# Optimization experiments

Measured on AMD Instinct MI355X. Metric: run time of the kernel, lower is better.

## Reference

```python
import jax, jax.numpy as jnp
import numpy as np

IMG_SIZE = 256
NUM_ANGLES = 180
NUM_DETECTORS = 363  # ceil(sqrt(2)*256)


def setup_inputs() -> dict:
    key = jax.random.key(0)
    x = jax.random.normal(key, (4, 1, IMG_SIZE, IMG_SIZE), dtype=jnp.float32)
    return {"x": x}


def _radon(x):
    # x: (B,1,H,W) -> sinogram (B,1,A,D). Faithful to RadonTransform.forward
    # (grid_sample rotate, sum rows, bilinear resize detector axis, align_corners=True).
    B, C, H, W = x.shape
    A, D = NUM_ANGLES, NUM_DETECTORS
    angles = jnp.linspace(0.0, np.pi * (1.0 - 1.0 / A), A, dtype=x.dtype)
    yc = jnp.linspace(-1.0, 1.0, H, dtype=x.dtype)
    xc = jnp.linspace(-1.0, 1.0, W, dtype=x.dtype)
    yy, xx = jnp.meshgrid(yc, xc, indexing='ij')          # (H,W)
    cos_t = jnp.cos(-angles)[:, None, None]               # (A,1,1)
    sin_t = jnp.sin(-angles)[:, None, None]
    gx = xx[None] * cos_t - yy[None] * sin_t              # (A,H,W) normalized x coord
    gy = xx[None] * sin_t + yy[None] * cos_t              # (A,H,W) normalized y coord
    # grid_sample bilinear, padding_mode='zeros', align_corners=True
    fx = (gx + 1.0) * 0.5 * (W - 1)
    fy = (gy + 1.0) * 0.5 * (H - 1)
    x0 = jnp.floor(fx).astype(jnp.int32); x1 = x0 + 1
    y0 = jnp.floor(fy).astype(jnp.int32); y1 = y0 + 1
    wx = fx - x0.astype(x.dtype)
    wy = fy - y0.astype(x.dtype)
    img = x[:, 0]                                         # (B,H,W)

    def tap(yi, xi):
        valid = (yi >= 0) & (yi < H) & (xi >= 0) & (xi < W)
        ycl = jnp.clip(yi, 0, H - 1)
        xcl = jnp.clip(xi, 0, W - 1)
        v = img[:, ycl, xcl]                              # (B,A,H,W)
        return jnp.where(valid[None], v, jnp.zeros((), x.dtype))

    sampled = (tap(y0, x0) * ((1 - wy) * (1 - wx))[None]
               + tap(y0, x1) * ((1 - wy) * wx)[None]
               + tap(y1, x0) * (wy * (1 - wx))[None]
               + tap(y1, x1) * (wy * wx)[None])           # (B,A,H,W)
    proj = sampled.sum(axis=2)                            # (B,A,W) sum along rows (dim=2)
    # F.interpolate to (A, D), bilinear, align_corners=True; angle axis is identity.
    pos = jnp.arange(D, dtype=x.dtype) * (W - 1) / (D - 1)
    p0 = jnp.floor(pos).astype(jnp.int32)
    p1 = jnp.minimum(p0 + 1, W - 1)
    w = pos - p0.astype(x.dtype)
    sino = proj[:, :, p0] * (1.0 - w) + proj[:, :, p1] * w  # (B,A,D)
    return sino[:, None]                                   # (B,1,A,D)


def reference(x):
    # CTForwardModel.forward(x, add_noise=False): noiseless sinogram = Radon(x)
    return _radon(x)
```

## Files before the change

### kernel.cpp

```cpp
#include <hip/hip_runtime.h>
#include <hip/hip_fp16.h>
#include <math.h>

#define IMG   256
#define NANG  180
#define NDET  363
#define PAD   3
#define PS    264
#define PSZ   (PS * PS)
#define TEX_BYTES ((size_t)2 * PSZ * 8)
#define PP_BYTES  ((size_t)NANG * 2 * IMG * 16)
#define WS_NEED   (TEX_BYTES + PP_BYTES)

__device__ __forceinline__ __half2 u2h2(unsigned u) {
    return *reinterpret_cast<__half2*>(&u);
}
__device__ __forceinline__ unsigned h22u(__half2 h) {
    return *reinterpret_cast<unsigned*>(&h);
}

__global__ __launch_bounds__(1024) void prep_kernel(const float* __restrict__ x,
                                                    uint2* __restrict__ ws) {
    __shared__ uint2 tile[32][33];
    const int tx = threadIdx.x, ty = threadIdx.y;
    const int px = blockIdx.x * 32 + tx;
    const int py = blockIdx.y * 32 + ty;
    const int ix = px - PAD, iy = py - PAD;

    uint2 t = make_uint2(0u, 0u);
    if ((unsigned)ix < IMG && (unsigned)iy < IMG) {
        const size_t o = (size_t)iy * IMG + ix;
        const __half2 lo = __floats2half2_rn(x[o],                 x[o + IMG * IMG]);
        const __half2 hi = __floats2half2_rn(x[o + 2 * IMG * IMG], x[o + 3 * IMG * IMG]);
        t.x = h22u(lo);
        t.y = h22u(hi);
    }
    if (px < PS && py < PS) ws[(size_t)py * PS + px] = t;
    tile[ty][tx] = t;
    __syncthreads();
    const int opx = blockIdx.y * 32 + tx;
    const int opy = blockIdx.x * 32 + ty;
    if (opx < PS && opy < PS)
        ws[(size_t)PSZ + (size_t)opy * PS + opx] = tile[tx][ty];
}

__global__ __launch_bounds__(512) void radon_main(const uint2* __restrict__ ws,
                                                  float4* __restrict__ proj_part) {
    const int a    = blockIdx.x;
    const int ih   = blockIdx.y >> 1;
    const int jh   = blockIdx.y & 1;
    const int lane = threadIdx.x & 63;
    const int wv   = threadIdx.x >> 6;
    const int jj   = lane & 15;
    const int ii4  = lane >> 4;
    const int j    = jh * 128 + wv * 16 + jj;

    const float ang = (float)a * 0.017453292519943295f;
    const float cs = cosf(ang);
    const float sn = -sinf(ang);

    const float xcj = -1.0f + (2.0f / 255.0f) * (float)j;
    const float fx0 = 127.5f * (xcj * cs + sn + 1.0f);
    const float dfx = -sn;
    const float fy0 = 127.5f * (xcj * sn - cs + 1.0f);
    const float dfy = cs;

    const bool swp = fabsf(sn) > fabsf(cs);
    const float rc0 = swp ? fx0 : fy0;  const float drow = swp ? dfx : dfy;
    const float cc0 = swp ? fy0 : fx0;  const float dcol = swp ? dfy : dfx;
    const uint2* __restrict__ base = ws + (swp ? PSZ : 0);

    float lo = 0.0f, hi = 255.0f;
    if (fabsf(drow) > 1e-5f) {
        const float t1 = (-1.5f - rc0) / drow, t2 = (256.5f - rc0) / drow;
        lo = fmaxf(lo, fminf(t1, t2));
        hi = fminf(hi, fmaxf(t1, t2));
    } else if (rc0 < -1.5f || rc0 > 256.5f) { lo = 1.0f; hi = 0.0f; }
    if (fabsf(dcol) > 1e-5f) {
        const float t1 = (-1.5f - cc0) / dcol, t2 = (256.5f - cc0) / dcol;
        lo = fmaxf(lo, fminf(t1, t2));
        hi = fminf(hi, fmaxf(t1, t2));
    } else if (cc0 < -1.5f || cc0 > 256.5f) { lo = 1.0f; hi = 0.0f; }

    const int ibase = ih * 128;
    int ilo_t = max((int)floorf(lo), ibase);
    int ihi_t = min((int)ceilf(hi), ibase + 127);
    ihi_t = min(ihi_t, 255);
    const int d0 = ilo_t - ibase - ii4;
    const int d1 = ihi_t - ibase - ii4;
    const int klo = max(0, (d0 + 3) >> 2);
    const int khi = min(31, d1 >> 2);

    float4 sum = make_float4(0.f, 0.f, 0.f, 0.f);
    #pragma unroll 4
    for (int k = klo; k <= khi; ++k) {
        const int i = ibase + ii4 + (k << 2);
        const float rc = fmaf((float)i, drow, rc0);
        const float cc = fmaf((float)i, dcol, cc0);
        const float rf = floorf(rc);
        const float cf = floorf(cc);
        const float wr = rc - rf;
        const float wc = cc - cf;
        const int idx = (int)fmaf(rf, (float)PS, cf) + (PAD * PS + PAD);

        const uint4 tr = *reinterpret_cast<const uint4*>(base + idx);
        const uint4 br = *reinterpret_cast<const uint4*>(base + idx + PS);

        const __half2 wc2 = __float2half2_rn(wc);
        const __half2 wr2 = __float2half2_rn(wr);

        const __half2 v00a = u2h2(tr.x), v00b = u2h2(tr.y);
        const __half2 v01a = u2h2(tr.z), v01b = u2h2(tr.w);
        const __half2 v10a = u2h2(br.x), v10b = u2h2(br.y);
        const __half2 v11a = u2h2(br.z), v11b = u2h2(br.w);

        const __half2 topa = __hfma2(wc2, __hsub2(v01a, v00a), v00a);
        const __half2 topb = __hfma2(wc2, __hsub2(v01b, v00b), v00b);
        const __half2 bota = __hfma2(wc2, __hsub2(v11a, v10a), v10a);
        const __half2 botb = __hfma2(wc2, __hsub2(v11b, v10b), v10b);
        const __half2 ra = __hfma2(wr2, __hsub2(bota, topa), topa);
        const __half2 rb = __hfma2(wr2, __hsub2(botb, topb), topb);

        sum.x += __low2float(ra);
        sum.y += __high2float(ra);
        sum.z += __low2float(rb);
        sum.w += __high2float(rb);
    }

    sum.x += __shfl_xor(sum.x, 16, 64);
    sum.y += __shfl_xor(sum.y, 16, 64);
    sum.z += __shfl_xor(sum.z, 16, 64);
    sum.w += __shfl_xor(sum.w, 16, 64);
    sum.x += __shfl_xor(sum.x, 32, 64);
    sum.y += __shfl_xor(sum.y, 32, 64);
    sum.z += __shfl_xor(sum.z, 32, 64);
    sum.w += __shfl_xor(sum.w, 32, 64);

    if (ii4 == 0) {
        proj_part[(size_t)(a * 2 + ih) * IMG + j] = sum;
    }
}

__global__ __launch_bounds__(384) void detect_kernel(const float4* __restrict__ proj_part,
                                                     float* __restrict__ out) {
    const int a = blockIdx.x;
    const int t = threadIdx.x;
    __shared__ float4 proj[IMG];
    if (t < IMG) {
        const float4 p0 = proj_part[(size_t)(a * 2 + 0) * IMG + t];
        const float4 p1 = proj_part[(size_t)(a * 2 + 1) * IMG + t];
        proj[t] = make_float4(p0.x + p1.x, p0.y + p1.y, p0.z + p1.z, p0.w + p1.w);
    }
    __syncthreads();
    if (t < NDET) {
        const float pos = (float)t * (255.0f / 362.0f);
        const float fp = floorf(pos);
        const int p0 = (int)fp;
        const int p1 = min(p0 + 1, IMG - 1);
        const float w = pos - fp;
        const float4 lo = proj[p0], hi = proj[p1];
        const size_t o = (size_t)a * NDET + t;
        out[o]                   = fmaf(w, hi.x - lo.x, lo.x);
        out[o + 1 * NANG * NDET] = fmaf(w, hi.y - lo.y, lo.y);
        out[o + 2 * NANG * NDET] = fmaf(w, hi.z - lo.z, lo.z);
        out[o + 3 * NANG * NDET] = fmaf(w, hi.w - lo.w, lo.w);
    }
}

__global__ __launch_bounds__(256) void radon_fallback(const float* __restrict__ x,
                                                      float* __restrict__ out) {
    const int blk = blockIdx.x;
    const int a = blk >> 2;
    const int b = blk & 3;
    const int j = threadIdx.x;
    const float* __restrict__ img = x + (size_t)b * (IMG * IMG);
    const float ang = (float)a * 0.017453292519943295f;
    const float cs = cosf(ang);
    const float sn = -sinf(ang);
    const float xcj = -1.0f + (2.0f / 255.0f) * (float)j;
    const float gx0 = xcj * cs;
    const float gy0 = xcj * sn;
    float sum = 0.0f;
    for (int i = 0; i < IMG; ++i) {
        const float yci = -1.0f + (2.0f / 255.0f) * (float)i;
        const float fx = (gx0 - yci * sn + 1.0f) * 127.5f;
        const float fy = (gy0 + yci * cs + 1.0f) * 127.5f;
        const float flx = floorf(fx), fly = floorf(fy);
        const int x0 = (int)flx, y0 = (int)fly;
        const float wx = fx - flx, wy = fy - fly;
        const bool vx0 = ((unsigned)x0 < IMG), vx1 = ((unsigned)(x0 + 1) < IMG);
        const bool vy0 = ((unsigned)y0 < IMG), vy1 = ((unsigned)(y0 + 1) < IMG);
        if (!((vx0 | vx1) & (vy0 | vy1))) continue;
        const int xc0 = min(max(x0, 0), IMG - 1), xc1 = min(max(x0 + 1, 0), IMG - 1);
        const int yc0 = min(max(y0, 0), IMG - 1), yc1 = min(max(y0 + 1, 0), IMG - 1);
        const float* r0 = img + yc0 * IMG;
        const float* r1 = img + yc1 * IMG;
        const float v00 = (vy0 && vx0) ? r0[xc0] : 0.0f;
        const float v01 = (vy0 && vx1) ? r0[xc1] : 0.0f;
        const float v10 = (vy1 && vx0) ? r1[xc0] : 0.0f;
        const float v11 = (vy1 && vx1) ? r1[xc1] : 0.0f;
        sum += (1.0f - wy) * ((1.0f - wx) * v00 + wx * v01)
             +         wy  * ((1.0f - wx) * v10 + wx * v11);
    }
    __shared__ float proj[IMG];
    proj[j] = sum;
    __syncthreads();
    for (int d = j; d < NDET; d += 256) {
        const float pos = (float)d * (255.0f / 362.0f);
        const float fp = floorf(pos);
        const int p0 = (int)fp;
        const int p1 = min(p0 + 1, IMG - 1);
        const float w = pos - fp;
        out[(size_t)b * (NANG * NDET) + a * NDET + d] = proj[p0] * (1.0f - w) + proj[p1] * w;
    }
}

extern "C" void kernel_launch(void* const* d_in, const int* in_sizes, int n_in,
                              void* d_out, int out_size, void* d_ws, size_t ws_size,
                              hipStream_t stream) {
    const float* x = (const float*)d_in[0];
    float* out = (float*)d_out;
    (void)in_sizes; (void)n_in; (void)out_size;

    if (ws_size >= WS_NEED) {
        uint2* tex = (uint2*)d_ws;
        float4* proj_part = (float4*)((char*)d_ws + TEX_BYTES);
        prep_kernel<<<dim3(9, 9), dim3(32, 32), 0, stream>>>(x, tex);
        radon_main<<<dim3(NANG, 4), dim3(512), 0, stream>>>(tex, proj_part);
        detect_kernel<<<dim3(NANG), dim3(384), 0, stream>>>(proj_part, out);
    } else {
        radon_fallback<<<dim3(NANG * 4), dim3(256), 0, stream>>>(x, out);
    }
}
```

Measured before the change: 31.42 us.

## Fuse prep, projection and detector stages into one cooperative kernel with grid syncs

Replaces the three-kernel sequence with a single cooperative kernel that runs texture preparation, the per-angle line integrals, and detector interpolation, separated by grid-wide syncs. The aim is to remove two kernel launch gaps and their inter-kernel drain/fill overhead. It adds a host occupancy query on every call and grid.sync costs, and falls back to the old three launches if cooperative launch is not possible.

```diff
diff --git a/kernel.cpp b/kernel.cpp
--- a/kernel.cpp
+++ b/kernel.cpp
@@ -1,6 +1,9 @@
 #include <hip/hip_runtime.h>
+#include <hip/hip_cooperative_groups.h>
 #include <hip/hip_fp16.h>
 #include <math.h>
+
+namespace cg = cooperative_groups;
 
 #define IMG   256
 #define NANG  180
@@ -19,38 +22,12 @@
     return *reinterpret_cast<unsigned*>(&h);
 }
 
-__global__ __launch_bounds__(1024) void prep_kernel(const float* __restrict__ x,
-                                                    uint2* __restrict__ ws) {
-    __shared__ uint2 tile[32][33];
-    const int tx = threadIdx.x, ty = threadIdx.y;
-    const int px = blockIdx.x * 32 + tx;
-    const int py = blockIdx.y * 32 + ty;
-    const int ix = px - PAD, iy = py - PAD;
-
-    uint2 t = make_uint2(0u, 0u);
-    if ((unsigned)ix < IMG && (unsigned)iy < IMG) {
-        const size_t o = (size_t)iy * IMG + ix;
-        const __half2 lo = __floats2half2_rn(x[o],                 x[o + IMG * IMG]);
-        const __half2 hi = __floats2half2_rn(x[o + 2 * IMG * IMG], x[o + 3 * IMG * IMG]);
-        t.x = h22u(lo);
-        t.y = h22u(hi);
-    }
-    if (px < PS && py < PS) ws[(size_t)py * PS + px] = t;
-    tile[ty][tx] = t;
-    __syncthreads();
-    const int opx = blockIdx.y * 32 + tx;
-    const int opy = blockIdx.x * 32 + ty;
-    if (opx < PS && opy < PS)
-        ws[(size_t)PSZ + (size_t)opy * PS + opx] = tile[tx][ty];
-}
-
-__global__ __launch_bounds__(512) void radon_main(const uint2* __restrict__ ws,
-                                                  float4* __restrict__ proj_part) {
-    const int a    = blockIdx.x;
-    const int ih   = blockIdx.y >> 1;
-    const int jh   = blockIdx.y & 1;
-    const int lane = threadIdx.x & 63;
-    const int wv   = threadIdx.x >> 6;
+
+__device__ __forceinline__ void main_phase(const uint2* __restrict__ ws,
+                                           float4* __restrict__ proj_part,
+                                           int a, int ih, int jh, int tid) {
+    const int lane = tid & 63;
+    const int wv   = tid >> 6;
     const int jj   = lane & 15;
     const int ii4  = lane >> 4;
     const int j    = jh * 128 + wv * 16 + jj;
@@ -83,7 +60,7 @@
     } else if (cc0 < -1.5f || cc0 > 256.5f) { lo = 1.0f; hi = 0.0f; }
 
     const int ibase = ih * 128;
-    int ilo_t = max((int)floorf(lo), ibase);
+    const int ilo_t = max((int)floorf(lo), ibase);
     int ihi_t = min((int)ceilf(hi), ibase + 127);
     ihi_t = min(ihi_t, 255);
     const int d0 = ilo_t - ibase - ii4;
@@ -139,6 +116,108 @@
     if (ii4 == 0) {
         proj_part[(size_t)(a * 2 + ih) * IMG + j] = sum;
     }
+}
+
+__global__ __launch_bounds__(512, 6) void radon_fused(const float* __restrict__ x,
+                                                      uint2* __restrict__ tex,
+                                                      float4* __restrict__ proj_part,
+                                                      float* __restrict__ out) {
+    cg::grid_group grid = cg::this_grid();
+    const int bid = blockIdx.x;
+    const int tid = threadIdx.x;
+
+    __shared__ uint2 s_tile[16][33];
+    __shared__ float4 s_proj[IMG];
+
+    if (bid < 9 * 17) {
+        const int bx = bid % 9, by = bid / 9;
+        const int tx = tid & 31, ty = tid >> 5;
+        const int px = bx * 32 + tx;
+        const int py = by * 16 + ty;
+        const int ix = px - PAD, iy = py - PAD;
+
+        uint2 t = make_uint2(0u, 0u);
+        if ((unsigned)ix < IMG && (unsigned)iy < IMG) {
+            const size_t o = (size_t)iy * IMG + ix;
+            const __half2 lo = __floats2half2_rn(x[o],                 x[o + IMG * IMG]);
+            const __half2 hi = __floats2half2_rn(x[o + 2 * IMG * IMG], x[o + 3 * IMG * IMG]);
+            t.x = h22u(lo);
+            t.y = h22u(hi);
+        }
+        if (px < PS && py < PS) tex[(size_t)py * PS + px] = t;
+        s_tile[ty][tx] = t;
+        __syncthreads();
+        const int u_local = tid >> 4;
+        const int v_local = tid & 15;
+        const int u = bx * 32 + u_local;
+        const int v = by * 16 + v_local;
+        if (u < PS && v < PS)
+            tex[(size_t)PSZ + (size_t)u * PS + v] = s_tile[v_local][u_local];
+    }
+
+    grid.sync();
+
+    {
+        const int a  = bid >> 2;
+        const int ih = (bid >> 1) & 1;
+        const int jh = bid & 1;
+        main_phase(tex, proj_part, a, ih, jh, tid);
+    }
+
+    grid.sync();
+
+    if (bid < NANG) {
+        const int a = bid;
+        if (tid < IMG) {
+            const float4 p0 = proj_part[(size_t)(a * 2 + 0) * IMG + tid];
+            const float4 p1 = proj_part[(size_t)(a * 2 + 1) * IMG + tid];
+            s_proj[tid] = make_float4(p0.x + p1.x, p0.y + p1.y, p0.z + p1.z, p0.w + p1.w);
+        }
+        __syncthreads();
+        if (tid < NDET) {
+            const float pos = (float)tid * (255.0f / 362.0f);
+            const float fp = floorf(pos);
+            const int p0 = (int)fp;
+            const int p1 = min(p0 + 1, IMG - 1);
+            const float w = pos - fp;
+            const float4 lo = s_proj[p0], hi = s_proj[p1];
+            const size_t o = (size_t)a * NDET + tid;
+            out[o]                   = fmaf(w, hi.x - lo.x, lo.x);
+            out[o + 1 * NANG * NDET] = fmaf(w, hi.y - lo.y, lo.y);
+            out[o + 2 * NANG * NDET] = fmaf(w, hi.z - lo.z, lo.z);
+            out[o + 3 * NANG * NDET] = fmaf(w, hi.w - lo.w, lo.w);
+        }
+    }
+}
+
+__global__ __launch_bounds__(1024) void prep_kernel(const float* __restrict__ x,
+                                                    uint2* __restrict__ ws) {
+    __shared__ uint2 tile[32][33];
+    const int tx = threadIdx.x, ty = threadIdx.y;
+    const int px = blockIdx.x * 32 + tx;
+    const int py = blockIdx.y * 32 + ty;
+    const int ix = px - PAD, iy = py - PAD;
+
+    uint2 t = make_uint2(0u, 0u);
+    if ((unsigned)ix < IMG && (unsigned)iy < IMG) {
+        const size_t o = (size_t)iy * IMG + ix;
+        const __half2 lo = __floats2half2_rn(x[o],                 x[o + IMG * IMG]);
+        const __half2 hi = __floats2half2_rn(x[o + 2 * IMG * IMG], x[o + 3 * IMG * IMG]);
+        t.x = h22u(lo);
+        t.y = h22u(hi);
+    }
+    if (px < PS && py < PS) ws[(size_t)py * PS + px] = t;
+    tile[ty][tx] = t;
+    __syncthreads();
+    const int opx = blockIdx.y * 32 + tx;
+    const int opy = blockIdx.x * 32 + ty;
+    if (opx < PS && opy < PS)
+        ws[(size_t)PSZ + (size_t)opy * PS + opx] = tile[tx][ty];
+}
+
+__global__ __launch_bounds__(512) void radon_main(const uint2* __restrict__ ws,
+                                                  float4* __restrict__ proj_part) {
+    main_phase(ws, proj_part, blockIdx.x, blockIdx.y >> 1, blockIdx.y & 1, threadIdx.x);
 }
 
 __global__ __launch_bounds__(384) void detect_kernel(const float4* __restrict__ proj_part,
@@ -222,13 +301,27 @@
     float* out = (float*)d_out;
     (void)in_sizes; (void)n_in; (void)out_size;
 
-    if (ws_size >= WS_NEED) {
-        uint2* tex = (uint2*)d_ws;
-        float4* proj_part = (float4*)((char*)d_ws + TEX_BYTES);
-        prep_kernel<<<dim3(9, 9), dim3(32, 32), 0, stream>>>(x, tex);
-        radon_main<<<dim3(NANG, 4), dim3(512), 0, stream>>>(tex, proj_part);
-        detect_kernel<<<dim3(NANG), dim3(384), 0, stream>>>(proj_part, out);
-    } else {
+    if (ws_size < WS_NEED) {
         radon_fallback<<<dim3(NANG * 4), dim3(256), 0, stream>>>(x, out);
-    }
-}
+        return;
+    }
+
+    uint2* tex = (uint2*)d_ws;
+    float4* proj_part = (float4*)((char*)d_ws + TEX_BYTES);
+
+    int blocksPerCU = 0;
+    hipError_t occ_err = hipOccupancyMaxActiveBlocksPerMultiprocessor(
+        &blocksPerCU, (const void*)radon_fused, 512, 0);
+
+    if (occ_err == hipSuccess && blocksPerCU * 256 >= NANG * 4) {
+        void* args[] = {(void*)&x, (void*)&tex, (void*)&proj_part, (void*)&out};
+        hipError_t err = hipLaunchCooperativeKernel((const void*)radon_fused,
+                                                    dim3(NANG * 4), dim3(512),
+                                                    args, 0, stream);
+        if (err == hipSuccess) return;
+    }
+
+    prep_kernel<<<dim3(9, 9), dim3(32, 32), 0, stream>>>(x, tex);
+    radon_main<<<dim3(NANG, 4), dim3(512), 0, stream>>>(tex, proj_part);
+    detect_kernel<<<dim3(NANG), dim3(384), 0, stream>>>(proj_part, out);
+}
```

Result: no change. 31.06 us (-1.2%).

## Stage rotated 32x32 output tiles' texture footprint in LDS before bilinear sampling

Applied to the files above, without the earlier changes.

Radon main kernel now assigns each 128-thread block a 32x32 (row, column) tile per angle. The block cooperatively copies the tile's rotated footprint (52x52 padded fp16x4 texels) from global memory into shared memory, then samples all four bilinear taps from LDS instead of issuing two 16-byte global loads per sample. This is meant to cut global/L2 traffic and latency for the gather. In exchange it launches 64 blocks per angle instead of 4, writes 8 partial projections per angle instead of 2, and makes the detector kernel sum 8 partials. It also risks LDS bank conflicts from the 8-byte gathers.

```diff
diff --git a/kernel.cpp b/kernel.cpp
--- a/kernel.cpp
+++ b/kernel.cpp
@@ -8,8 +8,10 @@
 #define PAD   3
 #define PS    264
 #define PSZ   (PS * PS)
+#define LR    52
+#define LC    52
 #define TEX_BYTES ((size_t)2 * PSZ * 8)
-#define PP_BYTES  ((size_t)NANG * 2 * IMG * 16)
+#define PP_BYTES  ((size_t)NANG * 8 * IMG * 16)
 #define WS_NEED   (TEX_BYTES + PP_BYTES)
 
 __device__ __forceinline__ __half2 u2h2(unsigned u) {
@@ -30,10 +32,8 @@
     uint2 t = make_uint2(0u, 0u);
     if ((unsigned)ix < IMG && (unsigned)iy < IMG) {
         const size_t o = (size_t)iy * IMG + ix;
-        const __half2 lo = __floats2half2_rn(x[o],                 x[o + IMG * IMG]);
-        const __half2 hi = __floats2half2_rn(x[o + 2 * IMG * IMG], x[o + 3 * IMG * IMG]);
-        t.x = h22u(lo);
-        t.y = h22u(hi);
+        t.x = h22u(__floats2half2_rn(x[o],                 x[o + IMG * IMG]));
+        t.y = h22u(__floats2half2_rn(x[o + 2 * IMG * IMG], x[o + 3 * IMG * IMG]));
     }
     if (px < PS && py < PS) ws[(size_t)py * PS + px] = t;
     tile[ty][tx] = t;
@@ -44,16 +44,18 @@
         ws[(size_t)PSZ + (size_t)opy * PS + opx] = tile[tx][ty];
 }
 
-__global__ __launch_bounds__(512) void radon_main(const uint2* __restrict__ ws,
+__global__ __launch_bounds__(128) void radon_main(const uint2* __restrict__ ws,
                                                   float4* __restrict__ proj_part) {
-    const int a    = blockIdx.x;
-    const int ih   = blockIdx.y >> 1;
-    const int jh   = blockIdx.y & 1;
-    const int lane = threadIdx.x & 63;
-    const int wv   = threadIdx.x >> 6;
+    const int a   = blockIdx.x;
+    const int it  = blockIdx.y >> 3;
+    const int jt  = blockIdx.y & 7;
+    const int i0  = it * 32, j0 = jt * 32;
+    const int tid = threadIdx.x;
+    const int lane = tid & 63;
+    const int w    = tid >> 6;
     const int jj   = lane & 15;
     const int ii4  = lane >> 4;
-    const int j    = jh * 128 + wv * 16 + jj;
+    const int j    = j0 + w * 16 + jj;
 
     const float ang = (float)a * 0.017453292519943295f;
     const float cs = cosf(ang);
@@ -68,7 +70,43 @@
     const bool swp = fabsf(sn) > fabsf(cs);
     const float rc0 = swp ? fx0 : fy0;  const float drow = swp ? dfx : dfy;
     const float cc0 = swp ? fy0 : fx0;  const float dcol = swp ? dfy : dfx;
-    const uint2* __restrict__ base = ws + (swp ? PSZ : 0);
+    const uint2* __restrict__ gtex = ws + (swp ? PSZ : 0);
+
+    const float fxb = 127.5f * (sn - cs + 1.0f);
+    const float fyb = 127.5f * (-sn - cs + 1.0f);
+    const float rb  = swp ? fxb : fyb;
+    const float cb  = swp ? fyb : fxb;
+    const float rjs = swp ? cs : sn;
+    const float cjs = swp ? sn : cs;
+
+    const float jr0 = (float)j0 * rjs,  jr1 = (float)(j0 + 31) * rjs;
+    const float ir0 = (float)i0 * drow, ir1 = (float)(i0 + 31) * drow;
+    const float jc0 = (float)j0 * cjs,  jc1 = (float)(j0 + 31) * cjs;
+    const float ic0 = (float)i0 * dcol, ic1 = (float)(i0 + 31) * dcol;
+    const float rmin_f = rb + fminf(jr0, jr1) + fminf(ir0, ir1);
+    const float cmin_f = cb + fminf(jc0, jc1) + fminf(ic0, ic1);
+
+    int rmin_p = (int)floorf(rmin_f) + PAD - 2;
+    rmin_p = min(max(rmin_p, 0), PS - LR);
+    int cmin_p = (int)floorf(cmin_f) + PAD - 2;
+    cmin_p = (min(max(cmin_p, 0), PS - LC)) & ~1;
+
+    __shared__ __align__(16) uint2 s_tile[LR * LC];
+    {
+        const uint4* __restrict__ g4 =
+            reinterpret_cast<const uint4*>(gtex + (size_t)rmin_p * PS + cmin_p);
+        uint4* s4 = reinterpret_cast<uint4*>(s_tile);
+        #pragma unroll
+        for (int t = 0; t < 11; ++t) {
+            const int idx = tid + t * 128;
+            if (idx < LR * (LC / 2)) {
+                const int r = idx / (LC / 2);
+                const int c = idx - r * (LC / 2);
+                s4[idx] = g4[(size_t)r * (PS / 2) + c];
+            }
+        }
+    }
+    __syncthreads();
 
     float lo = 0.0f, hi = 255.0f;
     if (fabsf(drow) > 1e-5f) {
@@ -82,49 +120,51 @@
         hi = fminf(hi, fmaxf(t1, t2));
     } else if (cc0 < -1.5f || cc0 > 256.5f) { lo = 1.0f; hi = 0.0f; }
 
-    const int ibase = ih * 128;
-    int ilo_t = max((int)floorf(lo), ibase);
-    int ihi_t = min((int)ceilf(hi), ibase + 127);
-    ihi_t = min(ihi_t, 255);
-    const int d0 = ilo_t - ibase - ii4;
-    const int d1 = ihi_t - ibase - ii4;
+    const int ilo_t = max((int)floorf(lo), i0);
+    const int ihi_t = min(min((int)ceilf(hi), i0 + 31), 255);
+    const int d0 = ilo_t - i0 - ii4;
+    const int d1 = ihi_t - i0 - ii4;
     const int klo = max(0, (d0 + 3) >> 2);
-    const int khi = min(31, d1 >> 2);
+    const int khi = min(7, d1 >> 2);
+
+    const int lbase = (PAD - rmin_p) * LC + (PAD - cmin_p);
 
     float4 sum = make_float4(0.f, 0.f, 0.f, 0.f);
-    #pragma unroll 4
+    #pragma unroll
     for (int k = klo; k <= khi; ++k) {
-        const int i = ibase + ii4 + (k << 2);
+        const int i = i0 + ii4 + (k << 2);
         const float rc = fmaf((float)i, drow, rc0);
         const float cc = fmaf((float)i, dcol, cc0);
         const float rf = floorf(rc);
         const float cf = floorf(cc);
         const float wr = rc - rf;
         const float wc = cc - cf;
-        const int idx = (int)fmaf(rf, (float)PS, cf) + (PAD * PS + PAD);
-
-        const uint4 tr = *reinterpret_cast<const uint4*>(base + idx);
-        const uint4 br = *reinterpret_cast<const uint4*>(base + idx + PS);
+        const int sidx = (int)rf * LC + (int)cf + lbase;
+
+        const uint2 t00 = s_tile[sidx];
+        const uint2 t01 = s_tile[sidx + 1];
+        const uint2 t10 = s_tile[sidx + LC];
+        const uint2 t11 = s_tile[sidx + LC + 1];
 
         const __half2 wc2 = __float2half2_rn(wc);
         const __half2 wr2 = __float2half2_rn(wr);
 
-        const __half2 v00a = u2h2(tr.x), v00b = u2h2(tr.y);
-        const __half2 v01a = u2h2(tr.z), v01b = u2h2(tr.w);
-        const __half2 v10a = u2h2(br.x), v10b = u2h2(br.y);
-        const __half2 v11a = u2h2(br.z), v11b = u2h2(br.w);
+        const __half2 v00a = u2h2(t00.x), v00b = u2h2(t00.y);
+        const __half2 v01a = u2h2(t01.x), v01b = u2h2(t01.y);
+        const __half2 v10a = u2h2(t10.x), v10b = u2h2(t10.y);
+        const __half2 v11a = u2h2(t11.x), v11b = u2h2(t11.y);
 
         const __half2 topa = __hfma2(wc2, __hsub2(v01a, v00a), v00a);
         const __half2 topb = __hfma2(wc2, __hsub2(v01b, v00b), v00b);
         const __half2 bota = __hfma2(wc2, __hsub2(v11a, v10a), v10a);
         const __half2 botb = __hfma2(wc2, __hsub2(v11b, v10b), v10b);
         const __half2 ra = __hfma2(wr2, __hsub2(bota, topa), topa);
-        const __half2 rb = __hfma2(wr2, __hsub2(botb, topb), topb);
+        const __half2 rb2 = __hfma2(wr2, __hsub2(botb, topb), topb);
 
         sum.x += __low2float(ra);
         sum.y += __high2float(ra);
-        sum.z += __low2float(rb);
-        sum.w += __high2float(rb);
+        sum.z += __low2float(rb2);
+        sum.w += __high2float(rb2);
     }
 
     sum.x += __shfl_xor(sum.x, 16, 64);
@@ -137,7 +177,7 @@
     sum.w += __shfl_xor(sum.w, 32, 64);
 
     if (ii4 == 0) {
-        proj_part[(size_t)(a * 2 + ih) * IMG + j] = sum;
+        proj_part[(size_t)(a * 8 + it) * IMG + j] = sum;
     }
 }
 
@@ -147,9 +187,13 @@
     const int t = threadIdx.x;
     __shared__ float4 proj[IMG];
     if (t < IMG) {
-        const float4 p0 = proj_part[(size_t)(a * 2 + 0) * IMG + t];
-        const float4 p1 = proj_part[(size_t)(a * 2 + 1) * IMG + t];
-        proj[t] = make_float4(p0.x + p1.x, p0.y + p1.y, p0.z + p1.z, p0.w + p1.w);
+        float4 s = proj_part[(size_t)(a * 8 + 0) * IMG + t];
+        #pragma unroll
+        for (int q = 1; q < 8; ++q) {
+            const float4 p = proj_part[(size_t)(a * 8 + q) * IMG + t];
+            s.x += p.x; s.y += p.y; s.z += p.z; s.w += p.w;
+        }
+        proj[t] = s;
     }
     __syncthreads();
     if (t < NDET) {
@@ -222,13 +266,15 @@
     float* out = (float*)d_out;
     (void)in_sizes; (void)n_in; (void)out_size;
 
-    if (ws_size >= WS_NEED) {
-        uint2* tex = (uint2*)d_ws;
-        float4* proj_part = (float4*)((char*)d_ws + TEX_BYTES);
-        prep_kernel<<<dim3(9, 9), dim3(32, 32), 0, stream>>>(x, tex);
-        radon_main<<<dim3(NANG, 4), dim3(512), 0, stream>>>(tex, proj_part);
-        detect_kernel<<<dim3(NANG), dim3(384), 0, stream>>>(proj_part, out);
-    } else {
+    if (ws_size < WS_NEED) {
         radon_fallback<<<dim3(NANG * 4), dim3(256), 0, stream>>>(x, out);
-    }
-}
+        return;
+    }
+
+    uint2* tex = (uint2*)d_ws;
+    float4* proj_part = (float4*)((char*)d_ws + TEX_BYTES);
+
+    prep_kernel<<<dim3(9, 9), dim3(32, 32), 0, stream>>>(x, tex);
+    radon_main<<<dim3(NANG, 64), dim3(128), 0, stream>>>(tex, proj_part);
+    detect_kernel<<<dim3(NANG), dim3(384), 0, stream>>>(proj_part, out);
+}
```

Measured after the change: 44.62 us. 1.42x slower.
